# Optimization experiments

Measured on AMD Instinct MI355X. Metric: run time of the kernel, lower is better.

The kernel has to match this reference:

```python
import jax, jax.numpy as jnp
import numpy as np

N = 100000      # nodes
E = 1600000     # edges
D_IN = 256
D_HID = 256
D_OUT = 256
DROP_P = 0.5


def setup_inputs() -> dict:
    key = jax.random.key(0)
    ks = jax.random.split(key, 10)
    s = 1.0 / np.sqrt(D_HID)
    return {
        "z": jax.random.normal(ks[0], (N, D_OUT), jnp.float32),
        "omega": jax.random.normal(ks[1], (N, D_IN), jnp.float32),
        "edge_index": jax.random.randint(ks[2], (2, E), 0, N, jnp.int32),
        "W_lin": jax.random.normal(ks[3], (D_IN, D_HID), jnp.float32) * s,
        "b_lin": jnp.zeros((D_HID,), jnp.float32),
        "W_g1": jax.random.normal(ks[4], (D_HID, D_HID), jnp.float32) * s,
        "b_g1": jnp.zeros((D_HID,), jnp.float32),
        "W_g2": jax.random.normal(ks[5], (D_HID, D_OUT), jnp.float32) * s,
        "b_g2": jnp.zeros((D_OUT,), jnp.float32),
        "mask1": jax.random.bernoulli(ks[6], 1.0 - DROP_P, (N, D_HID)),
        "mask2": jax.random.bernoulli(ks[7], 1.0 - DROP_P, (N, D_HID)),
    }


def _gcn_norm(edge_index):
    # add self-loops, symmetric normalization deg^-1/2 * deg^-1/2
    loop = jnp.arange(N, dtype=edge_index.dtype)
    src = jnp.concatenate([edge_index[0], loop])
    dst = jnp.concatenate([edge_index[1], loop])
    deg = jax.ops.segment_sum(jnp.ones_like(dst, jnp.float32), dst, num_segments=N)
    dinv = jax.lax.rsqrt(deg)  # deg >= 1 because of self-loops
    norm = dinv[src] * dinv[dst]  # [E+N]
    return src, dst, norm


def _gcn_conv(x, W, b, src, dst, norm):
    h = x @ W                                  # [N, d_out]
    msg = h[src] * norm[:, None]               # gather over edges
    out = jax.ops.segment_sum(msg, dst, num_segments=N)  # scatter-add
    return out + b


def _dropout(x, mask):
    return jnp.where(mask, x * (1.0 / (1.0 - DROP_P)), 0.0)


def reference(z, omega, edge_index, W_lin, b_lin, W_g1, b_g1, W_g2, b_g2, mask1, mask2):
    src, dst, norm = _gcn_norm(edge_index)
    # layer 0: Linear + relu + dropout
    h = _dropout(jax.nn.relu(omega @ W_lin + b_lin), mask1)
    # layer 1: GCNConv + relu + dropout
    h = _dropout(jax.nn.relu(_gcn_conv(h, W_g1, b_g1, src, dst, norm)), mask2)
    # layer 2: GCNConv
    h = _gcn_conv(h, W_g2, b_g2, src, dst, norm)
    return z * h
```

## Files before the change

### kernel.cpp

```cpp
#include <hip/hip_runtime.h>
#include <stdint.h>

#define NN 100000
#define EE 1600000
#define DD 256

typedef __bf16 bf16;
typedef __attribute__((ext_vector_type(8))) __bf16 bf16x8;
typedef __attribute__((ext_vector_type(4))) float f32x4;
typedef __attribute__((ext_vector_type(4))) unsigned int u32x4;
typedef __attribute__((ext_vector_type(8))) unsigned short u16x8;

typedef __attribute__((address_space(1))) const unsigned int g_u32c;
typedef __attribute__((address_space(3))) unsigned int lds_u32;

__device__ __forceinline__ float bflo(unsigned int u) {
    union { unsigned int u; float f; } x; x.u = u << 16; return x.f;
}
__device__ __forceinline__ float bfhi(unsigned int u) {
    union { unsigned int u; float f; } x; x.u = u & 0xFFFF0000u; return x.f;
}
__device__ __forceinline__ unsigned short f2bf(float f) {
    return __builtin_bit_cast(unsigned short, (__bf16)f);
}

__global__ void count_deg_k(const int* __restrict__ dst, int* __restrict__ cnt) {
    int e = blockIdx.x * 256 + threadIdx.x;
    if (e < EE) atomicAdd(&cnt[dst[e]], 1);
}
__global__ __launch_bounds__(256) void scan_blk_k(const int* __restrict__ cnt,
                                                  int* __restrict__ part,
                                                  int* __restrict__ bsum,
                                                  float* __restrict__ dinv) {
    __shared__ int buf[256];
    int i = blockIdx.x * 256 + threadIdx.x;
    int v = 0;
    if (i < NN) { v = cnt[i] + 1; dinv[i] = rsqrtf((float)v); }
    buf[threadIdx.x] = v;
    __syncthreads();
    for (int off = 1; off < 256; off <<= 1) {
        int t = (threadIdx.x >= off) ? buf[threadIdx.x - off] : 0;
        __syncthreads();
        buf[threadIdx.x] += t;
        __syncthreads();
    }
    if (i < NN) part[i] = buf[threadIdx.x];
    if (threadIdx.x == 255) bsum[blockIdx.x] = buf[255];
}
__global__ __launch_bounds__(512) void scan_top_k(const int* __restrict__ bsum,
                                                  int* __restrict__ bpre, int nb) {
    __shared__ int buf[512];
    int v = (threadIdx.x < (unsigned)nb) ? bsum[threadIdx.x] : 0;
    buf[threadIdx.x] = v;
    __syncthreads();
    for (int off = 1; off < 512; off <<= 1) {
        int t = (threadIdx.x >= off) ? buf[threadIdx.x - off] : 0;
        __syncthreads();
        buf[threadIdx.x] += t;
        __syncthreads();
    }
    if (threadIdx.x < (unsigned)nb) bpre[threadIdx.x] = buf[threadIdx.x] - v;
}
__global__ void scan_fin_k(const int* __restrict__ part, const int* __restrict__ bpre,
                           const int* __restrict__ cnt,
                           int* __restrict__ offs, int* __restrict__ cur,
                           int* __restrict__ cs) {
    int i = blockIdx.x * 256 + threadIdx.x;
    if (i >= NN) return;
    int o1 = part[i] + bpre[blockIdx.x];
    offs[i + 1] = o1;
    if (i == 0) offs[0] = 0;
    int o = o1 - (cnt[i] + 1);
    cs[o] = i;
    cur[i] = o + 1;
}
#define NSUB 128
__global__ __launch_bounds__(256) void fill_csr_k(
    const int* __restrict__ src, const int* __restrict__ dst,
    int* __restrict__ cur, int* __restrict__ cs) {
    int bid = blockIdx.x;
    int prt = bid & 7;
    int sub = bid >> 3;
    int lo = prt * (NN >> 3);
    int hi = (prt == 7) ? NN : lo + (NN >> 3);
    const int per = EE / NSUB;
    int e0 = sub * per;
    int e1 = (sub == NSUB - 1) ? EE : e0 + per;
    for (int e = e0 + threadIdx.x; e < e1; e += 256) {
        int d = dst[e];
        if (d >= lo && d < hi) {
            int s = src[e];
            int pos = atomicAdd(&cur[d], 1);
            cs[pos] = s;
        }
    }
}

__global__ __launch_bounds__(256) void prep_k(
    const float* __restrict__ W0, const float* __restrict__ W1, const float* __restrict__ W2,
    bf16* __restrict__ T0, bf16* __restrict__ T1, bf16* __restrict__ T2,
    const unsigned int* __restrict__ m, int* __restrict__ flag) {
    int b = blockIdx.x;
    if (b == 192) {
        if (threadIdx.x < 64) {
            unsigned int v = m[threadIdx.x];
            int bad = (v > 1u && v != 0x3F800000u) ? 1 : 0;
            unsigned long long bl = __ballot(bad);
            if (threadIdx.x == 0) *flag = (bl != 0ull) ? 1 : 0;
        }
        return;
    }
    const float* W = b < 64 ? W0 : (b < 128 ? W1 : W2);
    bf16*       T  = b < 64 ? T0 : (b < 128 ? T1 : T2);
    int bb = b & 63;
    __shared__ float tile[32][33];
    int bx = bb & 7, by = bb >> 3;
    int tx = threadIdx.x & 31, ty = threadIdx.x >> 5;
    #pragma unroll
    for (int r = 0; r < 32; r += 8)
        tile[ty + r][tx] = W[(size_t)(by * 32 + ty + r) * DD + bx * 32 + tx];
    __syncthreads();
    #pragma unroll
    for (int r = 0; r < 32; r += 8)
        T[(size_t)(bx * 32 + ty + r) * DD + by * 32 + tx] = (bf16)tile[tx][ty + r];
}

template <int ID, int EPI, int F32A>
__global__ __launch_bounds__(256) void gemm_k(
    const void* __restrict__ Ap, const bf16* __restrict__ Wt,
    const float* __restrict__ bias, const void* __restrict__ mask,
    const int* __restrict__ flagp, const float* __restrict__ z,
    const float* __restrict__ dinv, void* __restrict__ outp) {
    __shared__ __align__(16) bf16 As[128 * 64];
    __shared__ __align__(16) bf16 Bs[128 * 64];

    int bid = blockIdx.x;
    int m   = ((bid >> 4) << 3) | (bid & 7);
    int h   = (bid >> 3) & 1;
    int m0  = m * 128, n0 = h * 128;
    if (m0 >= NN) return;
    int tid = threadIdx.x;
    int wid = tid >> 6, lane = tid & 63;
    int wm = wid >> 1, wn = wid & 1;
    int lr = lane & 15, lk = lane >> 4;

    f32x4 acc[4][4] = {};

    for (int k0 = 0; k0 < DD; k0 += 64) {
        #pragma unroll
        for (int i = 0; i < 4; i++) {
            int f = i * 256 + tid;
            int row = f >> 3;
            int c   = (f & 7) * 8;
            int gr = m0 + row; if (gr > NN - 1) gr = NN - 1;
            if (F32A) {
                const float* sp = (const float*)Ap + (size_t)gr * DD + k0 + c;
                float4 v0 = *(const float4*)sp;
                float4 v1 = *(const float4*)(sp + 4);
                u16x8 o = { f2bf(v0.x), f2bf(v0.y), f2bf(v0.z), f2bf(v0.w),
                            f2bf(v1.x), f2bf(v1.y), f2bf(v1.z), f2bf(v1.w) };
                *(u16x8*)(As + row * 64 + c) = o;
            } else {
                __builtin_amdgcn_global_load_lds(
                    (g_u32c*)((const bf16*)Ap + (size_t)gr * DD + k0 + c),
                    (lds_u32*)(As + (size_t)f * 8), 16, 0, 0);
            }
            __builtin_amdgcn_global_load_lds(
                (g_u32c*)(Wt + (size_t)(n0 + row) * DD + k0 + c),
                (lds_u32*)(Bs + (size_t)f * 8), 16, 0, 0);
        }
        __syncthreads();
        #pragma unroll
        for (int kk = 0; kk < 2; kk++) {
            bf16x8 af[4], bfr[4];
            #pragma unroll
            for (int mi = 0; mi < 4; mi++)
                af[mi] = *(const bf16x8*)(As + (wm * 64 + mi * 16 + lr) * 64 + kk * 32 + lk * 8);
            #pragma unroll
            for (int ni = 0; ni < 4; ni++)
                bfr[ni] = *(const bf16x8*)(Bs + (wn * 64 + ni * 16 + lr) * 64 + kk * 32 + lk * 8);
            #pragma unroll
            for (int mi = 0; mi < 4; mi++)
                #pragma unroll
                for (int ni = 0; ni < 4; ni++)
                    acc[mi][ni] = __builtin_amdgcn_mfma_f32_16x16x32_bf16(
                        bfr[ni], af[mi], acc[mi][ni], 0, 0, 0);
        }
        __syncthreads();
    }

    int bm = (EPI == 1) ? *flagp : 0;
    #pragma unroll
    for (int mi = 0; mi < 4; mi++) {
        int gr = m0 + wm * 64 + mi * 16 + lr;
        if (gr >= NN) continue;
        float ds = (EPI == 1) ? dinv[gr] : 0.f;
        #pragma unroll
        for (int ni = 0; ni < 4; ni++) {
            int gc = n0 + wn * 64 + ni * 16 + lk * 4;
            size_t idx = (size_t)gr * DD + gc;
            float4 b4 = *(const float4*)(bias + gc);
            float v0 = acc[mi][ni][0] + b4.x;
            float v1 = acc[mi][ni][1] + b4.y;
            float v2 = acc[mi][ni][2] + b4.z;
            float v3 = acc[mi][ni][3] + b4.w;
            if (EPI == 1) {
                v0 = fmaxf(v0, 0.f); v1 = fmaxf(v1, 0.f);
                v2 = fmaxf(v2, 0.f); v3 = fmaxf(v3, 0.f);
                if (bm) {
                    uchar4 u = *(const uchar4*)((const unsigned char*)mask + idx);
                    v0 *= u.x ? 2.f : 0.f; v1 *= u.y ? 2.f : 0.f;
                    v2 *= u.z ? 2.f : 0.f; v3 *= u.w ? 2.f : 0.f;
                } else {
                    uint4 u = *(const uint4*)((const unsigned int*)mask + idx);
                    v0 *= u.x ? 2.f : 0.f; v1 *= u.y ? 2.f : 0.f;
                    v2 *= u.z ? 2.f : 0.f; v3 *= u.w ? 2.f : 0.f;
                }
                v0 *= ds; v1 *= ds; v2 *= ds; v3 *= ds;
                ushort4 o = { f2bf(v0), f2bf(v1), f2bf(v2), f2bf(v3) };
                *(ushort4*)((unsigned short*)outp + idx) = o;
            } else {
                f32x4 zz = __builtin_nontemporal_load((const f32x4*)(z + idx));
                f32x4 o = { v0 * zz.x, v1 * zz.y, v2 * zz.z, v3 * zz.w };
                __builtin_nontemporal_store(o, (f32x4*)((float*)outp + idx));
            }
        }
    }
}

#define AGG_GET(J, UVAR, MVAR)                                                   \
    {                                                                            \
        int _i = 2 * (J) + half;                                                 \
        int _s = __shfl(sl, _i & 63);                                            \
        MVAR = (_i < nume) ? 1.f : 0.f;                                          \
        UVAR = *(const u32x4*)(tb + (((size_t)(unsigned)_s) << 9) + lcoff);      \
    }
#define AGG_FMA(UVAR, MVAR)                                                      \
    {                                                                            \
        acc[0] = fmaf(MVAR, bflo(UVAR.x), acc[0]);                               \
        acc[1] = fmaf(MVAR, bfhi(UVAR.x), acc[1]);                               \
        acc[2] = fmaf(MVAR, bflo(UVAR.y), acc[2]);                               \
        acc[3] = fmaf(MVAR, bfhi(UVAR.y), acc[3]);                               \
        acc[4] = fmaf(MVAR, bflo(UVAR.z), acc[4]);                               \
        acc[5] = fmaf(MVAR, bfhi(UVAR.z), acc[5]);                               \
        acc[6] = fmaf(MVAR, bflo(UVAR.w), acc[6]);                               \
        acc[7] = fmaf(MVAR, bfhi(UVAR.w), acc[7]);                               \
    }

__global__ __launch_bounds__(256) void agg_k(
    const bf16* __restrict__ t, const int* __restrict__ offs,
    const int* __restrict__ cs, const float* __restrict__ dinv,
    bf16* __restrict__ out) {
    int node = blockIdx.x * 4 + (threadIdx.x >> 6);
    if (node >= NN) return;
    int lane = threadIdx.x & 63;
    int half = lane >> 5;
    int lc = lane & 31;
    int beg = offs[node], end = offs[node + 1];

    float acc[8] = {};
    const char* tb = (const char*)t;
    size_t lcoff = (size_t)(lc << 4);

    for (int base = beg; base < end; base += 64) {
        int nume = min(64, end - base);
        int sl = 0;
        if (lane < nume) sl = __builtin_nontemporal_load(cs + base + lane);
        int nit = (nume + 1) >> 1;

        u32x4 ua, ub, uc, ud;
        float ma, mb, mc, md;
        AGG_GET(0, ua, ma);
        AGG_GET(1, ub, mb);
        AGG_GET(2, uc, mc);
        int j = 0;
        for (; j + 3 < nit; j += 4) {
            AGG_GET(j + 3, ud, md); AGG_FMA(ua, ma);
            AGG_GET(j + 4, ua, ma); AGG_FMA(ub, mb);
            AGG_GET(j + 5, ub, mb); AGG_FMA(uc, mc);
            AGG_GET(j + 6, uc, mc); AGG_FMA(ud, md);
        }
        int rem = nit - j;
        if (rem > 0) AGG_FMA(ua, ma);
        if (rem > 1) AGG_FMA(ub, mb);
        if (rem > 2) AGG_FMA(uc, mc);
    }

    float dn = dinv[node];
    #pragma unroll
    for (int i = 0; i < 8; i++) {
        acc[i] += __shfl_xor(acc[i], 32);
        acc[i] *= dn;
    }
    if (half == 0) {
        u16x8 o = { f2bf(acc[0]), f2bf(acc[1]), f2bf(acc[2]), f2bf(acc[3]),
                    f2bf(acc[4]), f2bf(acc[5]), f2bf(acc[6]), f2bf(acc[7]) };
        __builtin_nontemporal_store(o, (u16x8*)((unsigned short*)out + (size_t)node * DD + lc * 8));
    }
}

extern "C" void kernel_launch(void* const* d_in, const int* in_sizes, int n_in,
                              void* d_out, int out_size, void* d_ws, size_t ws_size,
                              hipStream_t stream) {
    const float* z     = (const float*)d_in[0];
    const float* omega = (const float*)d_in[1];
    const int*   eidx  = (const int*)d_in[2];
    const float* W_lin = (const float*)d_in[3];
    const float* b_lin = (const float*)d_in[4];
    const float* W_g1  = (const float*)d_in[5];
    const float* b_g1  = (const float*)d_in[6];
    const float* W_g2  = (const float*)d_in[7];
    const float* b_g2  = (const float*)d_in[8];
    const void*  mask1 = d_in[9];
    const void*  mask2 = d_in[10];

    const int* e_src = eidx;
    const int* e_dst = eidx + EE;

    char* p = (char*)d_ws;
    size_t off = 0;
    auto alloc = [&](size_t bytes) -> char* {
        char* r = p + off;
        off = (off + bytes + 255) & ~(size_t)255;
        return r;
    };
    const int NB256 = (NN + 255) / 256;
    int*   flag = (int*)  alloc(4);
    int*   cnt  = (int*)  alloc((size_t)NN * 4);
    int*   offs = (int*)  alloc(((size_t)NN + 1) * 4);
    int*   cur  = (int*)  alloc((size_t)NN * 4);
    int*   part = (int*)  alloc((size_t)NN * 4);
    int*   bsum = (int*)  alloc(512 * 4);
    int*   bpre = (int*)  alloc(512 * 4);
    float* dinv = (float*)alloc((size_t)NN * 4);
    int*   cs   = (int*)  alloc((size_t)(EE + NN) * 4);
    bf16*  WtL  = (bf16*) alloc((size_t)DD * DD * 2);
    bf16*  Wt1  = (bf16*) alloc((size_t)DD * DD * 2);
    bf16*  Wt2  = (bf16*) alloc((size_t)DD * DD * 2);
    const size_t NBH = (size_t)NN * DD * 2;
    bf16*  S1   = (bf16*) alloc(NBH);
    bf16*  S2   = (bf16*) alloc(NBH);

    (void)hipMemsetAsync(cnt, 0, (size_t)NN * 4, stream);
    count_deg_k<<<EE / 256, 256, 0, stream>>>(e_dst, cnt);
    scan_blk_k <<<NB256, 256, 0, stream>>>(cnt, part, bsum, dinv);
    scan_top_k <<<1, 512, 0, stream>>>(bsum, bpre, NB256);
    scan_fin_k <<<NB256, 256, 0, stream>>>(part, bpre, cnt, offs, cur, cs);
    fill_csr_k <<<NSUB * 8, 256, 0, stream>>>(e_src, e_dst, cur, cs);

    prep_k<<<193, 256, 0, stream>>>(W_lin, W_g1, W_g2, WtL, Wt1, Wt2,
                                    (const unsigned int*)mask1, flag);

    const int GG = 1568;
    gemm_k<0, 1, 1><<<GG, 256, 0, stream>>>(omega, WtL, b_lin, mask1, flag, nullptr, dinv, S1);
    agg_k<<<NN / 4, 256, 0, stream>>>(S1, offs, cs, dinv, S2);
    gemm_k<1, 1, 0><<<GG, 256, 0, stream>>>(S2, Wt1, b_g1, mask2, flag, nullptr, dinv, S1);
    agg_k<<<NN / 4, 256, 0, stream>>>(S1, offs, cs, dinv, S2);
    gemm_k<2, 2, 0><<<GG, 256, 0, stream>>>(S2, Wt2, b_g2, nullptr, flag, z, dinv, d_out);
}
```

Before: 619.4 us.

## Use 64x256 GEMM tiles and partition degree counting by destination range

The GEMM tile changes from 128x128 to 64 rows by the full 256 columns, so each input row block is loaded and, for the fp32 first layer, converted only once instead of twice. Each warp now owns a 64-column slice, and the whole W^T chunk for every k-step is staged in LDS. The degree-count kernel is restructured like fill_csr: blocks split edges into sub-ranges and destination-node partitions, which localizes the atomics. The cost is that every count block rereads its share of dst eight times, and the GEMM runs fewer, larger-LDS blocks with more B traffic per block.

```diff
diff --git a/kernel.cpp b/kernel.cpp
--- a/kernel.cpp
+++ b/kernel.cpp
@@ -24,9 +24,21 @@
     return __builtin_bit_cast(unsigned short, (__bf16)f);
 }
 
-__global__ void count_deg_k(const int* __restrict__ dst, int* __restrict__ cnt) {
-    int e = blockIdx.x * 256 + threadIdx.x;
-    if (e < EE) atomicAdd(&cnt[dst[e]], 1);
+#define NSUB 128
+__global__ __launch_bounds__(256) void count_deg_k(
+    const int* __restrict__ dst, int* __restrict__ cnt) {
+    int bid = blockIdx.x;
+    int prt = bid & 7;
+    int sub = bid >> 3;
+    int lo = prt * (NN >> 3);
+    int hi = (prt == 7) ? NN : lo + (NN >> 3);
+    const int per = EE / NSUB;
+    int e0 = sub * per;
+    int e1 = (sub == NSUB - 1) ? EE : e0 + per;
+    for (int e = e0 + threadIdx.x; e < e1; e += 256) {
+        int d = dst[e];
+        if (d >= lo && d < hi) atomicAdd(&cnt[d], 1);
+    }
 }
 __global__ __launch_bounds__(256) void scan_blk_k(const int* __restrict__ cnt,
                                                   int* __restrict__ part,
@@ -74,7 +86,6 @@
     cs[o] = i;
     cur[i] = o + 1;
 }
-#define NSUB 128
 __global__ __launch_bounds__(256) void fill_csr_k(
     const int* __restrict__ src, const int* __restrict__ dst,
     int* __restrict__ cur, int* __restrict__ cs) {
@@ -131,24 +142,20 @@
     const float* __restrict__ bias, const void* __restrict__ mask,
     const int* __restrict__ flagp, const float* __restrict__ z,
     const float* __restrict__ dinv, void* __restrict__ outp) {
-    __shared__ __align__(16) bf16 As[128 * 64];
-    __shared__ __align__(16) bf16 Bs[128 * 64];
-
-    int bid = blockIdx.x;
-    int m   = ((bid >> 4) << 3) | (bid & 7);
-    int h   = (bid >> 3) & 1;
-    int m0  = m * 128, n0 = h * 128;
+    __shared__ __align__(16) bf16 As[64 * 64];
+    __shared__ __align__(16) bf16 Bs[256 * 64];
+
+    int m0 = blockIdx.x * 64;
     if (m0 >= NN) return;
     int tid = threadIdx.x;
     int wid = tid >> 6, lane = tid & 63;
-    int wm = wid >> 1, wn = wid & 1;
     int lr = lane & 15, lk = lane >> 4;
 
     f32x4 acc[4][4] = {};
 
     for (int k0 = 0; k0 < DD; k0 += 64) {
         #pragma unroll
-        for (int i = 0; i < 4; i++) {
+        for (int i = 0; i < 2; i++) {
             int f = i * 256 + tid;
             int row = f >> 3;
             int c   = (f & 7) * 8;
@@ -165,8 +172,14 @@
                     (g_u32c*)((const bf16*)Ap + (size_t)gr * DD + k0 + c),
                     (lds_u32*)(As + (size_t)f * 8), 16, 0, 0);
             }
+        }
+        #pragma unroll
+        for (int i = 0; i < 8; i++) {
+            int f = i * 256 + tid;
+            int row = f >> 3;
+            int c   = (f & 7) * 8;
             __builtin_amdgcn_global_load_lds(
-                (g_u32c*)(Wt + (size_t)(n0 + row) * DD + k0 + c),
+                (g_u32c*)(Wt + (size_t)row * DD + k0 + c),
                 (lds_u32*)(Bs + (size_t)f * 8), 16, 0, 0);
         }
         __syncthreads();
@@ -175,10 +188,10 @@
             bf16x8 af[4], bfr[4];
             #pragma unroll
             for (int mi = 0; mi < 4; mi++)
-                af[mi] = *(const bf16x8*)(As + (wm * 64 + mi * 16 + lr) * 64 + kk * 32 + lk * 8);
+                af[mi] = *(const bf16x8*)(As + (mi * 16 + lr) * 64 + kk * 32 + lk * 8);
             #pragma unroll
             for (int ni = 0; ni < 4; ni++)
-                bfr[ni] = *(const bf16x8*)(Bs + (wn * 64 + ni * 16 + lr) * 64 + kk * 32 + lk * 8);
+                bfr[ni] = *(const bf16x8*)(Bs + (wid * 64 + ni * 16 + lr) * 64 + kk * 32 + lk * 8);
             #pragma unroll
             for (int mi = 0; mi < 4; mi++)
                 #pragma unroll
@@ -192,12 +205,12 @@
     int bm = (EPI == 1) ? *flagp : 0;
     #pragma unroll
     for (int mi = 0; mi < 4; mi++) {
-        int gr = m0 + wm * 64 + mi * 16 + lr;
+        int gr = m0 + mi * 16 + lr;
         if (gr >= NN) continue;
         float ds = (EPI == 1) ? dinv[gr] : 0.f;
         #pragma unroll
         for (int ni = 0; ni < 4; ni++) {
-            int gc = n0 + wn * 64 + ni * 16 + lk * 4;
+            int gc = wid * 64 + ni * 16 + lk * 4;
             size_t idx = (size_t)gr * DD + gc;
             float4 b4 = *(const float4*)(bias + gc);
             float v0 = acc[mi][ni][0] + b4.x;
@@ -342,7 +355,7 @@
     bf16*  S2   = (bf16*) alloc(NBH);
 
     (void)hipMemsetAsync(cnt, 0, (size_t)NN * 4, stream);
-    count_deg_k<<<EE / 256, 256, 0, stream>>>(e_dst, cnt);
+    count_deg_k<<<NSUB * 8, 256, 0, stream>>>(e_dst, cnt);
     scan_blk_k <<<NB256, 256, 0, stream>>>(cnt, part, bsum, dinv);
     scan_top_k <<<1, 512, 0, stream>>>(bsum, bpre, NB256);
     scan_fin_k <<<NB256, 256, 0, stream>>>(part, bpre, cnt, offs, cur, cs);
@@ -351,10 +364,10 @@
     prep_k<<<193, 256, 0, stream>>>(W_lin, W_g1, W_g2, WtL, Wt1, Wt2,
                                     (const unsigned int*)mask1, flag);
 
-    const int GG = 1568;
-    gemm_k<0, 1, 1><<<GG, 256, 0, stream>>>(omega, WtL, b_lin, mask1, flag, nullptr, dinv, S1);
+    const int GB = (NN + 63) / 64;
+    gemm_k<0, 1, 1><<<GB, 256, 0, stream>>>(omega, WtL, b_lin, mask1, flag, nullptr, dinv, S1);
     agg_k<<<NN / 4, 256, 0, stream>>>(S1, offs, cs, dinv, S2);
-    gemm_k<1, 1, 0><<<GG, 256, 0, stream>>>(S2, Wt1, b_g1, mask2, flag, nullptr, dinv, S1);
+    gemm_k<1, 1, 0><<<GB, 256, 0, stream>>>(S2, Wt1, b_g1, mask2, flag, nullptr, dinv, S1);
     agg_k<<<NN / 4, 256, 0, stream>>>(S1, offs, cs, dinv, S2);
-    gemm_k<2, 2, 0><<<GG, 256, 0, stream>>>(S2, Wt2, b_g2, nullptr, flag, z, dinv, d_out);
-}
+    gemm_k<2, 2, 0><<<GB, 256, 0, stream>>>(S2, Wt2, b_g2, nullptr, flag, z, dinv, d_out);
+}
```

After: 611.3 us. About the same (-1.3%).
